# Optimization experiments

Measured on AMD Instinct MI355X. Metric: run time of the kernel, lower is better.

Reference implementation:

```python
import jax, jax.numpy as jnp
import numpy as np

B, S, D, H, Dh, F, L, V = 16, 512, 512, 8, 64, 2048, 6, 32000


def _layer_norm(x, g, b):
    m = x.mean(-1, keepdims=True)
    v = ((x - m) ** 2).mean(-1, keepdims=True)
    return (x - m) / jnp.sqrt(v + 1e-5) * g + b


def setup_inputs() -> dict:
    key = jax.random.key(0)
    ks = jax.random.split(key, 18)
    s = 0.02
    x = jax.random.randint(ks[0], (B, S), 0, V)
    batch_length = jax.random.randint(ks[1], (B,), 0, S)
    embed = (jax.random.normal(ks[2], (V, D)) * s).at[0].set(0.0)  # padding_idx=0 row zeroed
    Wq = jax.random.normal(ks[3], (L, D, H * Dh)) * s
    Wk = jax.random.normal(ks[4], (L, D, H * Dh)) * s
    Wv = jax.random.normal(ks[5], (L, D, H * Dh)) * s
    Wo = jax.random.normal(ks[6], (L, H * Dh, D)) * s
    bo = jnp.zeros((L, D))
    ln1_g = jnp.ones((L, D)); ln1_b = jnp.zeros((L, D))
    W1 = jax.random.normal(ks[7], (L, D, F)) * s
    b1 = jnp.zeros((L, F))
    W2 = jax.random.normal(ks[8], (L, F, D)) * s
    b2 = jnp.zeros((L, D))
    ln2_g = jnp.ones((L, D)); ln2_b = jnp.zeros((L, D))
    return dict(x=x, batch_length=batch_length, embed=embed, Wq=Wq, Wk=Wk, Wv=Wv,
                Wo=Wo, bo=bo, ln1_g=ln1_g, ln1_b=ln1_b, W1=W1, b1=b1, W2=W2,
                b2=b2, ln2_g=ln2_g, ln2_b=ln2_b)


def reference(x, batch_length, embed, Wq, Wk, Wv, Wo, bo, ln1_g, ln1_b,
              W1, b1, W2, b2, ln2_g, ln2_b):
    # sinusoidal positional encoding, exact replication (2.0*i/d with full index i)
    pos = jnp.arange(S, dtype=jnp.float32)[:, None]
    i = jnp.arange(D, dtype=jnp.float32)[None, :]
    ang = pos / jnp.power(10000.0, 2.0 * i / D)
    pe = ang.at[:, 0::2].set(jnp.sin(ang[:, 0::2])).at[:, 1::2].set(jnp.cos(ang[:, 1::2]))
    # per-sample PE truncated at batch_length (rest zero)
    len_mask = (jnp.arange(S)[None, :] < batch_length[:, None]).astype(pe.dtype)
    h = embed[x] + pe[None, :, :] * len_mask[:, :, None]  # [B,S,D]
    # padding mask: True where token==0, expanded to [B,S,S]; torch repeat(H,1,1) -> heads major
    pad = (x == 0)
    pmask = jnp.broadcast_to(pad[:, None, :], (B, S, S))
    mrep = jnp.tile(pmask, (H, 1, 1))  # [H*B, S, S], faithful to torch .repeat
    scale = 1.0 / np.sqrt(Dh).astype(np.float32)
    for l in range(L):
        # faithful .view(B*H, -1, Dh) on [B,S,H*Dh] contiguous memory
        q = (h @ Wq[l]).reshape(B * H, S, Dh)
        k = (h @ Wk[l]).reshape(B * H, S, Dh)
        v = (h @ Wv[l]).reshape(B * H, S, Dh)
        att = jnp.einsum('bqd,bkd->bqk', q, k) * scale  # [B*H,S,S]
        att = jnp.where(mrep, -1e9, att)
        att = jax.nn.softmax(att, axis=2)
        ctx = (att @ v).reshape(B, S, H * Dh)
        o = ctx @ Wo[l] + bo[l]
        h = _layer_norm(h + o, ln1_g[l], ln1_b[l])
        f = jax.nn.relu(h @ W1[l] + b1[l]) @ W2[l] + b2[l]
        h = _layer_norm(h + f, ln2_g[l], ln2_b[l])
    return h
```

## Files before the change

### kernel.cpp

```cpp
#include <hip/hip_runtime.h>
#include <hip/hip_bf16.h>
#include <cmath>

#define B_  16
#define S_  512
#define D_  512
#define F_  2048
#define L_  6
#define MT  8192

typedef __attribute__((ext_vector_type(8))) __bf16 bf16x8;
typedef __attribute__((ext_vector_type(4))) float  f32x4;

__device__ __forceinline__ unsigned short f2bf(float f) {
  return __builtin_bit_cast(unsigned short, __float2bfloat16(f));
}

__device__ __forceinline__ void gload16(const void* g, void* l) {
  __builtin_amdgcn_global_load_lds(
      (const __attribute__((address_space(1))) void*)g,
      (__attribute__((address_space(3))) void*)l, 16, 0, 0);
}

__global__ void embed_pe_kernel(const int* __restrict__ x,
                                const int* __restrict__ blen,
                                const float* __restrict__ emb,
                                float* __restrict__ h,
                                unsigned short* __restrict__ hbf) {
  int bs = blockIdx.x;
  int b = bs >> 9, s = bs & 511;
  int tok = x[bs];
  bool pe = s < blen[b];
  const float* er = emb + (long)tok * D_;
  long rb = (long)bs * D_;
  for (int d = threadIdx.x; d < D_; d += 256) {
    float e = er[d];
    if (pe) {
      float ex = (2.0f * (float)d) / 512.0f;
      float ang = (float)s / powf(10000.0f, ex);
      e += (d & 1) ? cosf(ang) : sinf(ang);
    }
    h[rb + d] = e;
    hbf[rb + d] = f2bf(e);
  }
}

__global__ void mask_build_kernel(const int* __restrict__ x,
                                  unsigned int* __restrict__ mw) {
  int t = threadIdx.x;
  int b = t >> 4, wd = t & 15;
  unsigned int m = 0;
  for (int j = 0; j < 32; j++)
    if (x[b * 512 + wd * 32 + j] == 0) m |= (1u << j);
  mw[b * 16 + wd] = m;
}

__global__ __launch_bounds__(256)
void wconv_kernel(const float* __restrict__ in, unsigned short* __restrict__ out,
                  int K, int N, long inls, long outls) {
  __shared__ float tile[32][33];
  const float* ip = in + (long)blockIdx.z * inls;
  unsigned short* op = out + (long)blockIdx.z * outls;
  int k0 = blockIdx.y * 32, n0 = blockIdx.x * 32;
  int tx = threadIdx.x & 31, ty = threadIdx.x >> 5;
  for (int i = ty; i < 32; i += 8) tile[i][tx] = ip[(long)(k0 + i) * N + n0 + tx];
  __syncthreads();
  for (int i = ty; i < 32; i += 8) op[(long)(n0 + i) * K + k0 + tx] = f2bf(tile[tx][i]);
}

template<int BMv, int MINW>
__global__ __launch_bounds__(256, MINW)
void gemm_bf16(const unsigned short* __restrict__ A,
               const unsigned short* __restrict__ Bt,
               const float* __restrict__ bias,
               float* __restrict__ C, unsigned short* __restrict__ Cbf,
               int M, int N, int K, int relu, int qkv) {
  constexpr int MFR = 4;
  constexpr int NFR = (BMv == 128) ? 4 : 2;
  __shared__ unsigned short Al[2][BMv * 32];
  __shared__ unsigned short Bl[2][128 * 32];
  int t = threadIdx.x;
  int lane = t & 63, wid = t >> 6;

  int flat = blockIdx.y * gridDim.x + blockIdx.x;
  int npx = (gridDim.x * gridDim.y) >> 3;
  int w = (flat & 7) * npx + (flat >> 3);
  int bx = w % gridDim.x, by = w / gridDim.x;

  int rbase = by * BMv, cbase = bx * 128;
  int wr = (BMv == 128) ? (wid >> 1) * 64 : 0;
  int wc = (BMv == 128) ? (wid & 1) * 64 : wid * 32;

  f32x4 acc[MFR][NFR];
#pragma unroll
  for (int i = 0; i < MFR; i++)
#pragma unroll
    for (int j = 0; j < NFR; j++) acc[i][j] = (f32x4){0.f, 0.f, 0.f, 0.f};

  int srow = t >> 2;
  int sc = (((t & 3) ^ ((t >> 3) & 3)) << 3);
  const unsigned short* Ag  = A  + (long)(rbase + srow) * K + sc;
  const unsigned short* Ag2 = A  + (long)(rbase + 64 + srow) * K + sc;
  const unsigned short* Bg  = Bt + (long)(cbase + srow) * K + sc;
  const unsigned short* Bg2 = Bt + (long)(cbase + 64 + srow) * K + sc;

  auto stage = [&](int bi, int kt) {
    gload16(Ag + kt, &Al[bi][t * 8]);
    if constexpr (BMv == 128) gload16(Ag2 + kt, &Al[bi][2048 + t * 8]);
    gload16(Bg + kt, &Bl[bi][t * 8]);
    gload16(Bg2 + kt, &Bl[bi][2048 + t * 8]);
  };

  int fr = lane & 15;
  int c4 = lane >> 4;

  int nt = K >> 5;
  stage(0, 0);
  int cur = 0;
  for (int tt = 0; tt < nt; ++tt) {
    if (tt + 1 < nt) {
      stage(cur ^ 1, (tt + 1) << 5);
      if constexpr (BMv == 128)
        asm volatile("s_waitcnt vmcnt(4)" ::: "memory");
      else
        asm volatile("s_waitcnt vmcnt(3)" ::: "memory");
    } else {
      asm volatile("s_waitcnt vmcnt(0)" ::: "memory");
    }
    __builtin_amdgcn_s_barrier();

    bf16x8 a[MFR], b[NFR];
#pragma unroll
    for (int m = 0; m < MFR; m++) {
      int R = wr + m * 16 + fr;
      a[m] = *(const bf16x8*)&Al[cur][R * 32 + ((c4 ^ ((R >> 1) & 3)) << 3)];
    }
#pragma unroll
    for (int n = 0; n < NFR; n++) {
      int R = wc + n * 16 + fr;
      b[n] = *(const bf16x8*)&Bl[cur][R * 32 + ((c4 ^ ((R >> 1) & 3)) << 3)];
    }
#pragma unroll
    for (int m = 0; m < MFR; m++)
#pragma unroll
      for (int n = 0; n < NFR; n++)
        acc[m][n] = __builtin_amdgcn_mfma_f32_16x16x32_bf16(a[m], b[n], acc[m][n], 0, 0, 0);
    __builtin_amdgcn_s_barrier();
    cur ^= 1;
  }

  if (BMv == 128 && qkv) {
#pragma unroll
    for (int m = 0; m < MFR; m++) {
#pragma unroll
      for (int n = 0; n < NFR; n++) {
        int col = cbase + wc + n * 16 + fr;
#pragma unroll
        for (int j = 0; j < 4; j++) {
          long row = rbase + wr + m * 16 + (lane >> 4) * 4 + j;
          unsigned short v = f2bf(acc[m][n][j]);
          if (col < 1024) {
            Cbf[(col < 512 ? 0L : 4194304L - 512L) + row * 512 + col] = v;
          } else {
            int cc = col - 1024;
            Cbf[8388608L + (row >> 6) * 32768 + (long)(cc & 63) * 512 +
                ((row & 63) << 3) + (cc >> 6)] = v;
          }
        }
      }
    }
  } else {
#pragma unroll
    for (int m = 0; m < MFR; m++) {
#pragma unroll
      for (int n = 0; n < NFR; n++) {
        int col = cbase + wc + n * 16 + fr;
        float bv = bias ? bias[col] : 0.0f;
#pragma unroll
        for (int j = 0; j < 4; j++) {
          long row = rbase + wr + m * 16 + (lane >> 4) * 4 + j;
          float v = acc[m][n][j] + bv;
          if (relu) v = fmaxf(v, 0.0f);
          if (C)   C[row * N + col] = v;
          if (Cbf) Cbf[row * N + col] = f2bf(v);
        }
      }
    }
  }
}

__global__ __launch_bounds__(256, 2)
void attn_mfma(const unsigned short* __restrict__ qbf,
               const unsigned short* __restrict__ kbf,
               const unsigned short* __restrict__ vtbf,
               const unsigned int* __restrict__ maskw,
               unsigned short* __restrict__ ctxbf) {
  __shared__ unsigned short sb[2][8192];
  int t = threadIdx.x;
  int lane = t & 63, w = t >> 6;
  int c = lane & 15, h = lane >> 4;

  int flat = blockIdx.y * 8 + blockIdx.x;
  int wk = (flat & 7) * 128 + (flat >> 3);
  int qt = wk & 7, bh = wk >> 3;

  long bhb = (long)bh << 15;
  int mb = bh & 15;

  const uint4* mp = (const uint4*)(maskw + mb * 16);
  uint4 m0 = mp[0], m1 = mp[1], m2 = mp[2], m3 = mp[3];
  unsigned int mwa[16] = {m0.x, m0.y, m0.z, m0.w, m1.x, m1.y, m1.z, m1.w,
                          m2.x, m2.y, m2.z, m2.w, m3.x, m3.y, m3.z, m3.w};

  const bf16x8* qp = (const bf16x8*)(qbf + bhb + (long)(qt * 64 + w * 16 + c) * 64);
  bf16x8 qf0 = qp[h], qf1 = qp[h + 4];

  auto stageK = [&](int bi, int ch) {
#pragma unroll
    for (int i = 0; i < 4; i++) {
      int idx = t + 256 * i;
      int kr = idx >> 3, g = idx & 7;
      gload16(kbf + bhb + (long)(ch * 128 + kr) * 64 + ((g ^ (kr & 7)) << 3),
              &sb[bi][idx * 8]);
    }
  };
  auto stageV = [&](int bi, int ch) {
#pragma unroll
    for (int i = 0; i < 4; i++) {
      int idx = t + 256 * i;
      int d = idx >> 4, g = idx & 15;
      gload16(vtbf + bhb + (long)d * 512 + ch * 128 + ((g ^ (d & 15)) << 3),
              &sb[bi][idx * 8]);
    }
  };

  f32x4 acc[32];
#pragma unroll
  for (int F = 0; F < 32; F++) acc[F] = (f32x4){0.f, 0.f, 0.f, 0.f};

  stageK(0, 0);
  int cur = 0;
#pragma unroll
  for (int ch = 0; ch < 4; ch++) {
    if (ch < 3) stageK(cur ^ 1, ch + 1);
    else        stageV(cur ^ 1, 0);
    asm volatile("s_waitcnt vmcnt(4)" ::: "memory");
    __builtin_amdgcn_s_barrier();
#pragma unroll
    for (int f = 0; f < 8; f++) {
      int R = f * 16 + c;
      int ro = R * 64;
      bf16x8 a0 = *(const bf16x8*)&sb[cur][ro + ((h ^ (R & 7)) << 3)];
      bf16x8 a1 = *(const bf16x8*)&sb[cur][ro + (((h + 4) ^ (R & 7)) << 3)];
      acc[ch * 8 + f] = __builtin_amdgcn_mfma_f32_16x16x32_bf16(a0, qf0, acc[ch * 8 + f], 0, 0, 0);
      acc[ch * 8 + f] = __builtin_amdgcn_mfma_f32_16x16x32_bf16(a1, qf1, acc[ch * 8 + f], 0, 0, 0);
    }
    __builtin_amdgcn_s_barrier();
    cur ^= 1;
  }

#pragma unroll
  for (int F = 0; F < 32; F++) {
    unsigned int nib = (mwa[F >> 1] >> (((F & 1) << 4) + (h << 2))) & 0xFu;
#pragma unroll
    for (int j = 0; j < 4; j++)
      acc[F][j] = (nib & (1u << j)) ? -1e9f : acc[F][j] * 0.125f;
  }

  float mx = -3.0e38f;
#pragma unroll
  for (int F = 0; F < 32; F++)
#pragma unroll
    for (int j = 0; j < 4; j++) mx = fmaxf(mx, acc[F][j]);
  mx = fmaxf(mx, __shfl_xor(mx, 16));
  mx = fmaxf(mx, __shfl_xor(mx, 32));
  float sm = 0.f;
#pragma unroll
  for (int F = 0; F < 32; F++)
#pragma unroll
    for (int j = 0; j < 4; j++) {
      float e = __expf(acc[F][j] - mx);
      acc[F][j] = e;
      sm += e;
    }
  sm += __shfl_xor(sm, 16);
  sm += __shfl_xor(sm, 32);

  unsigned int pk[64];
#pragma unroll
  for (int F = 0; F < 32; F++) {
    pk[2 * F]     = (unsigned int)f2bf(acc[F][0]) | ((unsigned int)f2bf(acc[F][1]) << 16);
    pk[2 * F + 1] = (unsigned int)f2bf(acc[F][2]) | ((unsigned int)f2bf(acc[F][3]) << 16);
  }

  float rs0 = 1.0f / __shfl(sm, h * 4 + 0);
  float rs1 = 1.0f / __shfl(sm, h * 4 + 1);
  float rs2 = 1.0f / __shfl(sm, h * 4 + 2);
  float rs3 = 1.0f / __shfl(sm, h * 4 + 3);

  f32x4 o[4];
#pragma unroll
  for (int n = 0; n < 4; n++) o[n] = (f32x4){0.f, 0.f, 0.f, 0.f};
  int l0 = c | ((lane & 16) << 1);
  int l1 = l0 + 16;
  bool hb = (lane & 32) != 0;

#pragma unroll
  for (int ch = 0; ch < 4; ch++) {
    if (ch < 3) {
      stageV(cur ^ 1, ch + 1);
      asm volatile("s_waitcnt vmcnt(4)" ::: "memory");
    } else {
      asm volatile("s_waitcnt vmcnt(0)" ::: "memory");
    }
    __builtin_amdgcn_s_barrier();
#pragma unroll
    for (int sub = 0; sub < 4; sub++) {
      int kt4 = (ch * 4 + sub) * 4;
      unsigned int a0 = __shfl((int)pk[kt4],     l0);
      unsigned int a1 = __shfl((int)pk[kt4 + 1], l0);
      unsigned int a2 = __shfl((int)pk[kt4],     l1);
      unsigned int a3 = __shfl((int)pk[kt4 + 1], l1);
      unsigned int b0 = __shfl((int)pk[kt4 + 2], l0);
      unsigned int b1 = __shfl((int)pk[kt4 + 3], l0);
      unsigned int b2 = __shfl((int)pk[kt4 + 2], l1);
      unsigned int b3 = __shfl((int)pk[kt4 + 3], l1);
      uint4 aw;
      aw.x = hb ? b0 : a0; aw.y = hb ? b1 : a1;
      aw.z = hb ? b2 : a2; aw.w = hb ? b3 : a3;
      bf16x8 af = __builtin_bit_cast(bf16x8, aw);
#pragma unroll
      for (int n = 0; n < 4; n++) {
        int dl = n * 16 + c;
        bf16x8 vf = *(const bf16x8*)&sb[cur][dl * 128 + (((sub * 4 + h) ^ (dl & 15)) << 3)];
        o[n] = __builtin_amdgcn_mfma_f32_16x16x32_bf16(af, vf, o[n], 0, 0, 0);
      }
    }
    __builtin_amdgcn_s_barrier();
    cur ^= 1;
  }

  unsigned short* cp = ctxbf + bhb + (long)(qt * 64 + w * 16) * 64;
#pragma unroll
  for (int n = 0; n < 4; n++) {
    cp[(h * 4 + 0) * 64 + n * 16 + c] = f2bf(o[n][0] * rs0);
    cp[(h * 4 + 1) * 64 + n * 16 + c] = f2bf(o[n][1] * rs1);
    cp[(h * 4 + 2) * 64 + n * 16 + c] = f2bf(o[n][2] * rs2);
    cp[(h * 4 + 3) * 64 + n * 16 + c] = f2bf(o[n][3] * rs3);
  }
}

__global__ __launch_bounds__(256)
void ln_kernel(const float* __restrict__ a, const float* __restrict__ r,
               const float* __restrict__ g, const float* __restrict__ be,
               float* __restrict__ out, unsigned short* __restrict__ outbf) {
  int w = threadIdx.x >> 6, lane = threadIdx.x & 63;
  long row = (long)blockIdx.x * 4 + w;
  long base = row * D_ + lane * 8;
  float4 a0 = *(const float4*)(a + base);
  float4 a1 = *(const float4*)(a + base + 4);
  float4 r0 = *(const float4*)(r + base);
  float4 r1 = *(const float4*)(r + base + 4);
  float xv[8] = {a0.x + r0.x, a0.y + r0.y, a0.z + r0.z, a0.w + r0.w,
                 a1.x + r1.x, a1.y + r1.y, a1.z + r1.z, a1.w + r1.w};
  float s = 0;
#pragma unroll
  for (int e = 0; e < 8; e++) s += xv[e];
#pragma unroll
  for (int off = 1; off < 64; off <<= 1) s += __shfl_xor(s, off);
  float m = s * (1.0f / 512.0f);
  float vs = 0;
#pragma unroll
  for (int e = 0; e < 8; e++) { float d = xv[e] - m; vs += d * d; }
#pragma unroll
  for (int off = 1; off < 64; off <<= 1) vs += __shfl_xor(vs, off);
  float rstd = 1.0f / sqrtf(vs * (1.0f / 512.0f) + 1e-5f);
  int gb = lane * 8;
  float o[8];
#pragma unroll
  for (int e = 0; e < 8; e++) o[e] = (xv[e] - m) * rstd * g[gb + e] + be[gb + e];
  *(float4*)(out + base)     = make_float4(o[0], o[1], o[2], o[3]);
  *(float4*)(out + base + 4) = make_float4(o[4], o[5], o[6], o[7]);
  ushort4 u0, u1;
  u0.x = f2bf(o[0]); u0.y = f2bf(o[1]); u0.z = f2bf(o[2]); u0.w = f2bf(o[3]);
  u1.x = f2bf(o[4]); u1.y = f2bf(o[5]); u1.z = f2bf(o[6]); u1.w = f2bf(o[7]);
  *(ushort4*)(outbf + base)     = u0;
  *(ushort4*)(outbf + base + 4) = u1;
}

extern "C" void kernel_launch(void* const* d_in, const int* in_sizes, int n_in,
                              void* d_out, int out_size, void* d_ws, size_t ws_size,
                              hipStream_t stream) {
  const int*   x    = (const int*)d_in[0];
  const int*   blen = (const int*)d_in[1];
  const float* emb  = (const float*)d_in[2];
  const float* Wq   = (const float*)d_in[3];
  const float* Wk   = (const float*)d_in[4];
  const float* Wv   = (const float*)d_in[5];
  const float* Wo   = (const float*)d_in[6];
  const float* bo   = (const float*)d_in[7];
  const float* ln1g = (const float*)d_in[8];
  const float* ln1b = (const float*)d_in[9];
  const float* W1   = (const float*)d_in[10];
  const float* b1   = (const float*)d_in[11];
  const float* W2   = (const float*)d_in[12];
  const float* b2   = (const float*)d_in[13];
  const float* ln2g = (const float*)d_in[14];
  const float* ln2b = (const float*)d_in[15];
  float* out = (float*)d_out;

  float* ws_f = (float*)d_ws;
  const long M4 = 4194304L;
  float* h   = ws_f;
  float* tmp = ws_f + M4;
  unsigned short* U = (unsigned short*)(ws_f + 2 * M4);
  unsigned short* h_bf   = U;
  unsigned short* q_bf   = U + M4;
  unsigned short* k_bf   = U + 2 * M4;
  unsigned short* vt_bf  = U + 3 * M4;
  unsigned short* ctx_bf = U + 4 * M4;
  unsigned short* mid_bf = q_bf;
  unsigned short* Wqkvt  = U + 5 * M4;
  unsigned short* Wot    = Wqkvt + 6L * 1536 * 512;
  unsigned short* W1t    = Wot   + 6L * 512 * 512;
  unsigned short* W2t    = W1t   + 6L * 2048 * 512;
  unsigned int*   maskw  = (unsigned int*)(W2t + 6L * 512 * 2048);

  wconv_kernel<<<dim3(16, 16, 6), 256, 0, stream>>>(Wq, Wqkvt,            512, 512,  262144L, 786432L);
  wconv_kernel<<<dim3(16, 16, 6), 256, 0, stream>>>(Wk, Wqkvt + 262144,   512, 512,  262144L, 786432L);
  wconv_kernel<<<dim3(16, 16, 6), 256, 0, stream>>>(Wv, Wqkvt + 524288,   512, 512,  262144L, 786432L);
  wconv_kernel<<<dim3(16, 16, 6), 256, 0, stream>>>(Wo, Wot,              512, 512,  262144L, 262144L);
  wconv_kernel<<<dim3(64, 16, 6), 256, 0, stream>>>(W1, W1t,              512, 2048, 1048576L, 1048576L);
  wconv_kernel<<<dim3(16, 64, 6), 256, 0, stream>>>(W2, W2t,              2048, 512, 1048576L, 1048576L);
  mask_build_kernel<<<1, 256, 0, stream>>>(x, maskw);
  embed_pe_kernel<<<MT, 256, 0, stream>>>(x, blen, emb, h, h_bf);

  dim3 gqkv(12, 64), g2048(16, 64), g512b(4, 128), gattn(8, 128);

  for (int l = 0; l < L_; l++) {
    const unsigned short* wqkv = Wqkvt + (long)l * 1536 * 512;
    const unsigned short* wo   = Wot   + (long)l * 512 * 512;
    const unsigned short* w1   = W1t   + (long)l * 2048 * 512;
    const unsigned short* w2   = W2t   + (long)l * 512 * 2048;

    gemm_bf16<128, 2><<<gqkv, 256, 0, stream>>>(h_bf, wqkv, nullptr, nullptr, q_bf,
                                                MT, 1536, 512, 0, 1);
    attn_mfma<<<gattn, 256, 0, stream>>>(q_bf, k_bf, vt_bf, maskw, ctx_bf);
    gemm_bf16<64, 3><<<g512b, 256, 0, stream>>>(ctx_bf, wo, bo + (long)l * D_, tmp, nullptr,
                                                MT, 512, 512, 0, 0);
    ln_kernel<<<MT / 4, 256, 0, stream>>>(h, tmp, ln1g + (long)l * D_,
                                          ln1b + (long)l * D_, h, h_bf);
    gemm_bf16<128, 2><<<g2048, 256, 0, stream>>>(h_bf, w1, b1 + (long)l * F_, nullptr, mid_bf,
                                                 MT, 2048, 512, 1, 0);
    gemm_bf16<64, 3><<<g512b, 256, 0, stream>>>(mid_bf, w2, b2 + (long)l * D_, tmp, nullptr,
                                                MT, 512, 2048, 0, 0);
    ln_kernel<<<MT / 4, 256, 0, stream>>>(h, tmp, ln2g + (long)l * D_,
                                          ln2b + (long)l * D_,
                                          (l == L_ - 1) ? out : h, h_bf);
  }
}
```

Baseline: 986.0 us.

## Convert attention to online softmax over key chunks to raise occupancy

Replaces the two-pass attention (full 512-key score matrix held in registers, then PV) with a flash-style online softmax that processes 128-key chunks, rescaling the running max, sum and output per chunk. This shrinks the per-thread score and packed-probability arrays from 32 fragments to 8, and the launch bounds are raised from 2 to 4 blocks per SIMD to turn the freed registers into occupancy. In exchange the K and V buffers become fixed slots staged with full __syncthreads barriers, so loads overlap less with compute, and each chunk adds extra exp and rescale work.

```diff
diff --git a/kernel.cpp b/kernel.cpp
--- a/kernel.cpp
+++ b/kernel.cpp
@@ -189,7 +189,7 @@
   }
 }
 
-__global__ __launch_bounds__(256, 2)
+__global__ __launch_bounds__(256, 4)
 void attn_mfma(const unsigned short* __restrict__ qbf,
                const unsigned short* __restrict__ kbf,
                const unsigned short* __restrict__ vtbf,
@@ -215,130 +215,124 @@
   const bf16x8* qp = (const bf16x8*)(qbf + bhb + (long)(qt * 64 + w * 16 + c) * 64);
   bf16x8 qf0 = qp[h], qf1 = qp[h + 4];
 
-  auto stageK = [&](int bi, int ch) {
+  auto stageK = [&](int ch) {
 #pragma unroll
     for (int i = 0; i < 4; i++) {
       int idx = t + 256 * i;
       int kr = idx >> 3, g = idx & 7;
       gload16(kbf + bhb + (long)(ch * 128 + kr) * 64 + ((g ^ (kr & 7)) << 3),
-              &sb[bi][idx * 8]);
+              &sb[0][idx * 8]);
     }
   };
-  auto stageV = [&](int bi, int ch) {
+  auto stageV = [&](int ch) {
 #pragma unroll
     for (int i = 0; i < 4; i++) {
       int idx = t + 256 * i;
       int d = idx >> 4, g = idx & 15;
       gload16(vtbf + bhb + (long)d * 512 + ch * 128 + ((g ^ (d & 15)) << 3),
-              &sb[bi][idx * 8]);
+              &sb[1][idx * 8]);
     }
   };
 
-  f32x4 acc[32];
-#pragma unroll
-  for (int F = 0; F < 32; F++) acc[F] = (f32x4){0.f, 0.f, 0.f, 0.f};
-
-  stageK(0, 0);
-  int cur = 0;
+  float m_run = -1e30f, sum_run = 0.0f;
+  f32x4 o[4];
+#pragma unroll
+  for (int n = 0; n < 4; n++) o[n] = (f32x4){0.f, 0.f, 0.f, 0.f};
+  int l0 = c | ((lane & 16) << 1);
+  int l1 = l0 + 16;
+  bool hb = (lane & 32) != 0;
+
+  stageK(0);
 #pragma unroll
   for (int ch = 0; ch < 4; ch++) {
-    if (ch < 3) stageK(cur ^ 1, ch + 1);
-    else        stageV(cur ^ 1, 0);
-    asm volatile("s_waitcnt vmcnt(4)" ::: "memory");
-    __builtin_amdgcn_s_barrier();
+    __syncthreads();
+    stageV(ch);
+
+    f32x4 acc[8];
+#pragma unroll
+    for (int f = 0; f < 8; f++) acc[f] = (f32x4){0.f, 0.f, 0.f, 0.f};
 #pragma unroll
     for (int f = 0; f < 8; f++) {
       int R = f * 16 + c;
       int ro = R * 64;
-      bf16x8 a0 = *(const bf16x8*)&sb[cur][ro + ((h ^ (R & 7)) << 3)];
-      bf16x8 a1 = *(const bf16x8*)&sb[cur][ro + (((h + 4) ^ (R & 7)) << 3)];
-      acc[ch * 8 + f] = __builtin_amdgcn_mfma_f32_16x16x32_bf16(a0, qf0, acc[ch * 8 + f], 0, 0, 0);
-      acc[ch * 8 + f] = __builtin_amdgcn_mfma_f32_16x16x32_bf16(a1, qf1, acc[ch * 8 + f], 0, 0, 0);
-    }
-    __builtin_amdgcn_s_barrier();
-    cur ^= 1;
-  }
-
-#pragma unroll
-  for (int F = 0; F < 32; F++) {
-    unsigned int nib = (mwa[F >> 1] >> (((F & 1) << 4) + (h << 2))) & 0xFu;
-#pragma unroll
-    for (int j = 0; j < 4; j++)
-      acc[F][j] = (nib & (1u << j)) ? -1e9f : acc[F][j] * 0.125f;
-  }
-
-  float mx = -3.0e38f;
-#pragma unroll
-  for (int F = 0; F < 32; F++)
-#pragma unroll
-    for (int j = 0; j < 4; j++) mx = fmaxf(mx, acc[F][j]);
-  mx = fmaxf(mx, __shfl_xor(mx, 16));
-  mx = fmaxf(mx, __shfl_xor(mx, 32));
-  float sm = 0.f;
-#pragma unroll
-  for (int F = 0; F < 32; F++)
-#pragma unroll
-    for (int j = 0; j < 4; j++) {
-      float e = __expf(acc[F][j] - mx);
-      acc[F][j] = e;
-      sm += e;
-    }
+      bf16x8 a0 = *(const bf16x8*)&sb[0][ro + ((h ^ (R & 7)) << 3)];
+      bf16x8 a1 = *(const bf16x8*)&sb[0][ro + (((h + 4) ^ (R & 7)) << 3)];
+      acc[f] = __builtin_amdgcn_mfma_f32_16x16x32_bf16(a0, qf0, acc[f], 0, 0, 0);
+      acc[f] = __builtin_amdgcn_mfma_f32_16x16x32_bf16(a1, qf1, acc[f], 0, 0, 0);
+    }
+
+#pragma unroll
+    for (int f = 0; f < 8; f++) {
+      unsigned int nib = (mwa[ch * 4 + (f >> 1)] >> (((f & 1) << 4) + (h << 2))) & 0xFu;
+#pragma unroll
+      for (int j = 0; j < 4; j++)
+        acc[f][j] = (nib & (1u << j)) ? -1e9f : acc[f][j] * 0.125f;
+    }
+
+    float cm = -3.0e38f;
+#pragma unroll
+    for (int f = 0; f < 8; f++)
+#pragma unroll
+      for (int j = 0; j < 4; j++) cm = fmaxf(cm, acc[f][j]);
+    cm = fmaxf(cm, __shfl_xor(cm, 16));
+    cm = fmaxf(cm, __shfl_xor(cm, 32));
+    float m_new = fmaxf(m_run, cm);
+    float scale = __expf(m_run - m_new);
+    m_run = m_new;
+#pragma unroll
+    for (int n = 0; n < 4; n++) o[n] *= scale;
+    float csum = 0.0f;
+#pragma unroll
+    for (int f = 0; f < 8; f++)
+#pragma unroll
+      for (int j = 0; j < 4; j++) {
+        float e = __expf(acc[f][j] - m_new);
+        acc[f][j] = e;
+        csum += e;
+      }
+    sum_run = sum_run * scale + csum;
+
+    unsigned int pkc[16];
+#pragma unroll
+    for (int f = 0; f < 8; f++) {
+      pkc[2 * f]     = (unsigned int)f2bf(acc[f][0]) | ((unsigned int)f2bf(acc[f][1]) << 16);
+      pkc[2 * f + 1] = (unsigned int)f2bf(acc[f][2]) | ((unsigned int)f2bf(acc[f][3]) << 16);
+    }
+
+    __syncthreads();
+    if (ch < 3) stageK(ch + 1);
+
+#pragma unroll
+    for (int sub = 0; sub < 4; sub++) {
+      int kt4 = sub * 4;
+      unsigned int a0 = __shfl((int)pkc[kt4],     l0);
+      unsigned int a1 = __shfl((int)pkc[kt4 + 1], l0);
+      unsigned int a2 = __shfl((int)pkc[kt4],     l1);
+      unsigned int a3 = __shfl((int)pkc[kt4 + 1], l1);
+      unsigned int b0 = __shfl((int)pkc[kt4 + 2], l0);
+      unsigned int b1 = __shfl((int)pkc[kt4 + 3], l0);
+      unsigned int b2 = __shfl((int)pkc[kt4 + 2], l1);
+      unsigned int b3 = __shfl((int)pkc[kt4 + 3], l1);
+      uint4 aw;
+      aw.x = hb ? b0 : a0; aw.y = hb ? b1 : a1;
+      aw.z = hb ? b2 : a2; aw.w = hb ? b3 : a3;
+      bf16x8 af = __builtin_bit_cast(bf16x8, aw);
+#pragma unroll
+      for (int n = 0; n < 4; n++) {
+        int dl = n * 16 + c;
+        bf16x8 vf = *(const bf16x8*)&sb[1][dl * 128 + (((sub * 4 + h) ^ (dl & 15)) << 3)];
+        o[n] = __builtin_amdgcn_mfma_f32_16x16x32_bf16(af, vf, o[n], 0, 0, 0);
+      }
+    }
+  }
+
+  float sm = sum_run;
   sm += __shfl_xor(sm, 16);
   sm += __shfl_xor(sm, 32);
-
-  unsigned int pk[64];
-#pragma unroll
-  for (int F = 0; F < 32; F++) {
-    pk[2 * F]     = (unsigned int)f2bf(acc[F][0]) | ((unsigned int)f2bf(acc[F][1]) << 16);
-    pk[2 * F + 1] = (unsigned int)f2bf(acc[F][2]) | ((unsigned int)f2bf(acc[F][3]) << 16);
-  }
-
   float rs0 = 1.0f / __shfl(sm, h * 4 + 0);
   float rs1 = 1.0f / __shfl(sm, h * 4 + 1);
   float rs2 = 1.0f / __shfl(sm, h * 4 + 2);
   float rs3 = 1.0f / __shfl(sm, h * 4 + 3);
-
-  f32x4 o[4];
-#pragma unroll
-  for (int n = 0; n < 4; n++) o[n] = (f32x4){0.f, 0.f, 0.f, 0.f};
-  int l0 = c | ((lane & 16) << 1);
-  int l1 = l0 + 16;
-  bool hb = (lane & 32) != 0;
-
-#pragma unroll
-  for (int ch = 0; ch < 4; ch++) {
-    if (ch < 3) {
-      stageV(cur ^ 1, ch + 1);
-      asm volatile("s_waitcnt vmcnt(4)" ::: "memory");
-    } else {
-      asm volatile("s_waitcnt vmcnt(0)" ::: "memory");
-    }
-    __builtin_amdgcn_s_barrier();
-#pragma unroll
-    for (int sub = 0; sub < 4; sub++) {
-      int kt4 = (ch * 4 + sub) * 4;
-      unsigned int a0 = __shfl((int)pk[kt4],     l0);
-      unsigned int a1 = __shfl((int)pk[kt4 + 1], l0);
-      unsigned int a2 = __shfl((int)pk[kt4],     l1);
-      unsigned int a3 = __shfl((int)pk[kt4 + 1], l1);
-      unsigned int b0 = __shfl((int)pk[kt4 + 2], l0);
-      unsigned int b1 = __shfl((int)pk[kt4 + 3], l0);
-      unsigned int b2 = __shfl((int)pk[kt4 + 2], l1);
-      unsigned int b3 = __shfl((int)pk[kt4 + 3], l1);
-      uint4 aw;
-      aw.x = hb ? b0 : a0; aw.y = hb ? b1 : a1;
-      aw.z = hb ? b2 : a2; aw.w = hb ? b3 : a3;
-      bf16x8 af = __builtin_bit_cast(bf16x8, aw);
-#pragma unroll
-      for (int n = 0; n < 4; n++) {
-        int dl = n * 16 + c;
-        bf16x8 vf = *(const bf16x8*)&sb[cur][dl * 128 + (((sub * 4 + h) ^ (dl & 15)) << 3)];
-        o[n] = __builtin_amdgcn_mfma_f32_16x16x32_bf16(af, vf, o[n], 0, 0, 0);
-      }
-    }
-    __builtin_amdgcn_s_barrier();
-    cur ^= 1;
-  }
 
   unsigned short* cp = ctxbf + bhb + (long)(qt * 64 + w * 16) * 64;
 #pragma unroll
```

New measurement: 1.096 ms. +11.1%, slower.
